# Kernel optimization log

Hardware: AMD Instinct MI355X
Metric: run time of the kernel (lower is better)

## Reference

```python
import jax, jax.numpy as jnp
import numpy as np

EPS = 1e-6


def layernorm(x, w, b):
    m = jnp.mean(x, axis=-1, keepdims=True)
    v = jnp.var(x, axis=-1, keepdims=True)
    return (x - m) * jax.lax.rsqrt(v + EPS) * w + b


def rotate_half(x):
    x1, x2 = jnp.split(x, 2, axis=-1)
    return jnp.concatenate((-x2, x1), axis=-1)


def setup_inputs() -> dict:
    key = jax.random.key(0)
    ks = jax.random.split(key, 16)
    T, D, H, HD, I = 16384, 1280, 16, 80, 5120
    NSEG = 16
    inp = {
        "hidden_states": jax.random.normal(ks[0], (T, D), jnp.float32),
        "cos": jax.random.uniform(ks[1], (T, HD), jnp.float32),
        "sin": jax.random.uniform(ks[2], (T, HD), jnp.float32),
        "ln1_w": jnp.ones((D,), jnp.float32),
        "ln1_b": jnp.zeros((D,), jnp.float32),
        "ln2_w": jnp.ones((D,), jnp.float32),
        "ln2_b": jnp.zeros((D,), jnp.float32),
        "qkv_w": jax.random.normal(ks[3], (3 * D, D), jnp.float32) * 0.02,
        "qkv_b": jnp.zeros((3 * D,), jnp.float32),
        "proj_w": jax.random.normal(ks[4], (D, D), jnp.float32) * 0.02,
        "proj_b": jnp.zeros((D,), jnp.float32),
        "fc1_w": jax.random.normal(ks[5], (I, D), jnp.float32) * 0.02,
        "fc1_b": jnp.zeros((I,), jnp.float32),
        "fc2_w": jax.random.normal(ks[6], (D, I), jnp.float32) * 0.02,
        "fc2_b": jnp.zeros((D,), jnp.float32),
        "cu_seqlens": jnp.arange(NSEG + 1, dtype=jnp.int32) * (T // NSEG),
    }
    return inp


def reference(hidden_states, cos, sin, ln1_w, ln1_b, ln2_w, ln2_b,
              qkv_w, qkv_b, proj_w, proj_b, fc1_w, fc1_b, fc2_w, fc2_b,
              cu_seqlens):
    T, D = hidden_states.shape
    H = 16
    HD = D // H
    nseg = cu_seqlens.shape[0] - 1  # equal-length segments by construction
    L = T // nseg

    x = layernorm(hidden_states, ln1_w, ln1_b)
    qkv = (x @ qkv_w.T + qkv_b).reshape(T, 3, H, HD)
    q, k, v = qkv[:, 0], qkv[:, 1], qkv[:, 2]  # [T, H, HD]

    # RoPE in fp32, cos/sin broadcast over heads
    c = cos[:, None, :]
    s = sin[:, None, :]
    q = q * c + rotate_half(q) * s
    k = k * c + rotate_half(k) * s

    # block-diagonal varlen attention: reshape into [nseg, L, H, HD]
    qs = q.reshape(nseg, L, H, HD)
    ks = k.reshape(nseg, L, H, HD)
    vs = v.reshape(nseg, L, H, HD)
    scale = 1.0 / jnp.sqrt(jnp.asarray(HD, jnp.float32))
    scores = jnp.einsum('slhd,smhd->shlm', qs, ks) * scale
    probs = jax.nn.softmax(scores, axis=-1)
    attn = jnp.einsum('shlm,smhd->slhd', probs, vs).reshape(T, D)

    attn_out = attn @ proj_w.T + proj_b
    h = hidden_states + attn_out

    y = layernorm(h, ln2_w, ln2_b)
    mlp = (jax.nn.silu(y @ fc1_w.T + fc1_b)) @ fc2_w.T + fc2_b
    return h + mlp
```

## Files before the change

### kernel.cpp

```cpp
#include <hip/hip_runtime.h>
#include <hip/hip_bf16.h>
#include <hip/hip_fp16.h>

typedef _Float16 f16;
typedef _Float16 f16x4 __attribute__((ext_vector_type(4)));
typedef _Float16 f16x8 __attribute__((ext_vector_type(8)));
typedef float f32x4 __attribute__((ext_vector_type(4)));

#define T_TOK 16384
#define D_MOD 1280
#define N_QKV 3840
#define I_MLP 5120
#define N_HEAD 16
#define HD 80
#define SEG_L 1024

__device__ __forceinline__ void async16(const void* g, void* l) {
    __builtin_amdgcn_global_load_lds(
        (const __attribute__((address_space(1))) void*)g,
        (__attribute__((address_space(3))) void*)l, 16, 0, 0);
}

__global__ __launch_bounds__(256) void cast_f32_f16(
    const float* __restrict__ src, f16* __restrict__ dst, int n) {
    int i = blockIdx.x * 256 + threadIdx.x;
    if (i < n) dst[i] = (f16)src[i];
}

template <typename TIN>
__global__ __launch_bounds__(256) void ln_kernel(
    const TIN* __restrict__ x, const float* __restrict__ w,
    const float* __restrict__ b, f16* __restrict__ out) {
    const int t = blockIdx.x;
    const TIN* row = x + (size_t)t * D_MOD;
    float vals[5];
    float s = 0.f, s2 = 0.f;
    for (int i = 0; i < 5; ++i) {
        float v = (float)row[threadIdx.x + i * 256];
        vals[i] = v; s += v; s2 += v * v;
    }
    for (int off = 32; off > 0; off >>= 1) {
        s  += __shfl_down(s, off);
        s2 += __shfl_down(s2, off);
    }
    __shared__ float rs[4], rs2[4];
    int wv = threadIdx.x >> 6;
    if ((threadIdx.x & 63) == 0) { rs[wv] = s; rs2[wv] = s2; }
    __syncthreads();
    s  = rs[0] + rs[1] + rs[2] + rs[3];
    s2 = rs2[0] + rs2[1] + rs2[2] + rs2[3];
    float m = s * (1.f / D_MOD);
    float var = s2 * (1.f / D_MOD) - m * m;
    float rstd = rsqrtf(var + 1e-6f);
    for (int i = 0; i < 5; ++i) {
        int c = threadIdx.x + i * 256;
        out[(size_t)t * D_MOD + c] = (f16)((vals[i] - m) * rstd * w[c] + b[c]);
    }
}

__global__ __launch_bounds__(256) void rope_inplace(
    f16* __restrict__ q, f16* __restrict__ k,
    const float* __restrict__ cosb, const float* __restrict__ sinb) {
    int i = blockIdx.x * 256 + threadIdx.x;
    if (i >= T_TOK * N_HEAD * 40) return;
    int d = i % 40;
    int th = i / 40;
    int h = th & 15;
    int t = th >> 4;
    size_t i0 = ((size_t)h * T_TOK + t) * HD + d;
    size_t i1 = i0 + 40;
    float c0 = cosb[t * HD + d],      s0 = sinb[t * HD + d];
    float c1 = cosb[t * HD + d + 40], s1 = sinb[t * HD + d + 40];
    {
        float x0 = (float)q[i0], x1 = (float)q[i1];
        q[i0] = (f16)(x0 * c0 - x1 * s0);
        q[i1] = (f16)(x1 * c1 + x0 * s1);
    }
    {
        float x0 = (float)k[i0], x1 = (float)k[i1];
        k[i0] = (f16)(x0 * c0 - x1 * s0);
        k[i1] = (f16)(x1 * c1 + x0 * s1);
    }
}

#define EPI_QKV   0
#define EPI_PROJ  1
#define EPI_SILU  2
#define EPI_FC2A  3
#define EPI_FC2B  4

template <int EPI>
__global__ __launch_bounds__(256, 2) void gemm_bt(
    const f16* __restrict__ A, const f16* __restrict__ B,
    const float* __restrict__ bias, const void* __restrict__ resid,
    void* __restrict__ out0, f16* __restrict__ out1, f16* __restrict__ out2,
    int M, int N, int K, int lda, int ldb, int ldo) {
    __shared__ f16 lA[128 * 32];
    __shared__ f16 lB[128 * 32];
    const int tid = threadIdx.x;
    const int w = tid >> 6, l = tid & 63;
    const int wr = w >> 1, wc = w & 1;
    const int lane16 = l & 15, quad = l >> 4;
    const int m0 = blockIdx.y * 128, n0 = blockIdx.x * 128;
    const int rowA = l >> 2;
    const int colA = (l & 3) * 8;

    f32x4 acc[4][4];
    for (int i = 0; i < 4; ++i)
        for (int j = 0; j < 4; ++j)
            acc[i][j] = (f32x4){0.f, 0.f, 0.f, 0.f};

    for (int k0 = 0; k0 < K; k0 += 32) {
        __syncthreads();
        for (int p = 0; p < 2; ++p) {
            int r = p * 64 + w * 16;
            async16(A + (size_t)(m0 + r + rowA) * lda + k0 + colA, &lA[r * 32]);
            async16(B + (size_t)(n0 + r + rowA) * ldb + k0 + colA, &lB[r * 32]);
        }
        __syncthreads();
        f16x8 af[4], bf[4];
        for (int i = 0; i < 4; ++i) {
            af[i] = *(const f16x8*)&lA[(wr * 64 + i * 16 + lane16) * 32 + quad * 8];
            bf[i] = *(const f16x8*)&lB[(wc * 64 + i * 16 + lane16) * 32 + quad * 8];
        }
        for (int mi = 0; mi < 4; ++mi)
            for (int ni = 0; ni < 4; ++ni)
                acc[mi][ni] = __builtin_amdgcn_mfma_f32_16x16x32_f16(
                    af[mi], bf[ni], acc[mi][ni], 0, 0, 0);
    }

    for (int mi = 0; mi < 4; ++mi) {
        int row = m0 + wr * 64 + mi * 16 + quad * 4;
        for (int ni = 0; ni < 4; ++ni) {
            int col = n0 + wc * 64 + ni * 16 + lane16;
            float bv = (EPI == EPI_FC2B) ? 0.f : bias[col];
            if (EPI == EPI_QKV) {
                int g = col / D_MOD;
                int rem = col - g * D_MOD;
                int h = rem / HD, d = rem - h * HD;
                if (g == 2) {
                    f16x4 pk;
                    for (int r2 = 0; r2 < 4; ++r2)
                        pk[r2] = (f16)(acc[mi][ni][r2] + bv);
                    f16* dst = out2 + ((size_t)h * HD + d) * T_TOK + row;
                    *(f16x4*)dst = pk;
                } else {
                    f16* dst = (g == 0) ? (f16*)out0 : out1;
                    size_t base = ((size_t)h * T_TOK) * HD + d;
                    for (int r2 = 0; r2 < 4; ++r2) {
                        float v = acc[mi][ni][r2] + bv;
                        dst[base + (size_t)(row + r2) * HD] = (f16)v;
                    }
                }
            } else {
                for (int r2 = 0; r2 < 4; ++r2) {
                    float v = acc[mi][ni][r2] + bv;
                    size_t idx = (size_t)(row + r2) * ldo + col;
                    if (EPI == EPI_PROJ) {
                        ((f16*)out0)[idx] = (f16)(v + ((const float*)resid)[idx]);
                    } else if (EPI == EPI_SILU) {
                        ((f16*)out0)[idx] = (f16)(v / (1.f + __expf(-v)));
                    } else if (EPI == EPI_FC2A) {
                        ((float*)out0)[idx] = v + (float)((const f16*)resid)[idx];
                    } else {
                        ((float*)out0)[idx] += v;
                    }
                }
            }
        }
    }
}

#define QK_STRIDE 104
#define VT_STRIDE 72
#define P_STRIDE  72
__global__ __launch_bounds__(256, 3) void attn_kernel(
    const f16* __restrict__ q, const f16* __restrict__ k,
    const f16* __restrict__ vt, f16* __restrict__ out) {
    const int bid = blockIdx.x;
    const int s = bid >> 8, h = (bid >> 4) & 15, qt = bid & 15;
    const int t0 = s * SEG_L;
    __shared__ f16 lQ[64 * QK_STRIDE];
    __shared__ f16 lK[64 * QK_STRIDE];
    __shared__ f16 lVt[80 * VT_STRIDE];
    __shared__ f16 lP[4 * 16 * P_STRIDE];
    const int tid = threadIdx.x;
    const int w = tid >> 6, l = tid & 63;
    const int lane16 = l & 15, quad = l >> 4;
    const f16 scale = (f16)0.16132167f;

    const f16* qbase  = q  + (size_t)h * T_TOK * HD + (size_t)(t0 + qt * 64) * HD;
    const f16* kbase  = k  + (size_t)h * T_TOK * HD + (size_t)t0 * HD;
    const f16* vtbase = vt + (size_t)h * HD * T_TOK + t0;

    for (int idx = tid; idx < 64 * 12; idx += 256) {
        int r = idx / 12, c8 = idx % 12;
        f16x8 val = (f16x8){0, 0, 0, 0, 0, 0, 0, 0};
        if (c8 < 10) {
            val = *(const f16x8*)&qbase[r * 80 + c8 * 8];
            val = val * scale;
        }
        *(f16x8*)&lQ[r * QK_STRIDE + c8 * 8] = val;
    }
    for (int idx = tid; idx < 64 * 2; idx += 256) {
        int r = idx >> 1, c8 = 10 + (idx & 1);
        *(f16x8*)&lK[r * QK_STRIDE + c8 * 8] = (f16x8){0, 0, 0, 0, 0, 0, 0, 0};
    }

    float lrow[4] = {0.f, 0.f, 0.f, 0.f};
    f32x4 o[5];
    for (int i = 0; i < 5; ++i) o[i] = (f32x4){0.f, 0.f, 0.f, 0.f};

    for (int kt = 0; kt < 16; ++kt) {
        __syncthreads();
        for (int idx = tid; idx < 64 * 10; idx += 256) {
            int r = idx / 10, c8 = idx % 10;
            *(f16x8*)&lK[r * QK_STRIDE + c8 * 8] =
                *(const f16x8*)&kbase[(kt * 64 + r) * 80 + c8 * 8];
        }
        for (int idx = tid; idx < 80 * 8; idx += 256) {
            int d = idx / 8, r8 = idx % 8;
            *(f16x8*)&lVt[d * VT_STRIDE + r8 * 8] =
                *(const f16x8*)&vtbase[(size_t)d * T_TOK + kt * 64 + r8 * 8];
        }
        __syncthreads();

        f32x4 sacc[4];
        for (int ct = 0; ct < 4; ++ct) {
            f32x4 a = (f32x4){0.f, 0.f, 0.f, 0.f};
            for (int ks = 0; ks < 3; ++ks) {
                f16x8 af = *(const f16x8*)&lQ[(w * 16 + lane16) * QK_STRIDE + ks * 32 + quad * 8];
                f16x8 bf = *(const f16x8*)&lK[(ct * 16 + lane16) * QK_STRIDE + ks * 32 + quad * 8];
                a = __builtin_amdgcn_mfma_f32_16x16x32_f16(af, bf, a, 0, 0, 0);
            }
            sacc[ct] = a;
        }

        for (int ct = 0; ct < 4; ++ct) {
            for (int r = 0; r < 4; ++r) {
                float p = __builtin_exp2f(fminf(sacc[ct][r], 14.f));
                lrow[r] += p;
                lP[w * 16 * P_STRIDE + (quad * 4 + r) * P_STRIDE + ct * 16 + lane16] = (f16)p;
            }
        }

        for (int vt2 = 0; vt2 < 5; ++vt2) {
            for (int ks = 0; ks < 2; ++ks) {
                f16x8 af = *(const f16x8*)&lP[w * 16 * P_STRIDE + lane16 * P_STRIDE + ks * 32 + quad * 8];
                f16x8 bf = *(const f16x8*)&lVt[(vt2 * 16 + lane16) * VT_STRIDE + ks * 32 + quad * 8];
                o[vt2] = __builtin_amdgcn_mfma_f32_16x16x32_f16(af, bf, o[vt2], 0, 0, 0);
            }
        }
    }

    for (int r = 0; r < 4; ++r)
        for (int off = 1; off < 16; off <<= 1)
            lrow[r] += __shfl_xor(lrow[r], off);

    f16* obase = out + (size_t)(t0 + qt * 64 + w * 16) * D_MOD + h * HD;
    for (int r = 0; r < 4; ++r) {
        float inv = 1.f / lrow[r];
        for (int vt2 = 0; vt2 < 5; ++vt2) {
            int row = quad * 4 + r;
            int hd = vt2 * 16 + lane16;
            obase[(size_t)row * D_MOD + hd] = (f16)(o[vt2][r] * inv);
        }
    }
}

extern "C" void kernel_launch(void* const* d_in, const int* in_sizes, int n_in,
                              void* d_out, int out_size, void* d_ws, size_t ws_size,
                              hipStream_t stream) {
    const float* hidden = (const float*)d_in[0];
    const float* cosb   = (const float*)d_in[1];
    const float* sinb   = (const float*)d_in[2];
    const float* ln1w   = (const float*)d_in[3];
    const float* ln1b   = (const float*)d_in[4];
    const float* ln2w   = (const float*)d_in[5];
    const float* ln2b   = (const float*)d_in[6];
    const float* qkvw   = (const float*)d_in[7];
    const float* qkvb   = (const float*)d_in[8];
    const float* projw  = (const float*)d_in[9];
    const float* projb  = (const float*)d_in[10];
    const float* fc1w   = (const float*)d_in[11];
    const float* fc1b   = (const float*)d_in[12];
    const float* fc2w   = (const float*)d_in[13];
    const float* fc2b   = (const float*)d_in[14];
    float* out = (float*)d_out;

    f16* wqkv  = (f16*)d_ws;
    f16* wproj = wqkv  + 4915200;
    f16* wfc1  = wproj + 1638400;
    f16* wfc2  = wfc1  + 6553600;
    f16* qf    = wfc2  + 6553600;
    f16* kf    = qf    + 20971520;
    f16* vf    = kf    + 20971520;
    f16* xf    = vf    + 20971520;
    f16* hbuf  = xf    + 20971520;
    f16* attnf  = xf;
    f16* yf     = qf;
    f16* fc1out = kf;

    cast_f32_f16<<<(4915200 + 255) / 256, 256, 0, stream>>>(qkvw, wqkv, 4915200);
    cast_f32_f16<<<(1638400 + 255) / 256, 256, 0, stream>>>(projw, wproj, 1638400);
    cast_f32_f16<<<(6553600 + 255) / 256, 256, 0, stream>>>(fc1w, wfc1, 6553600);
    cast_f32_f16<<<(6553600 + 255) / 256, 256, 0, stream>>>(fc2w, wfc2, 6553600);

    ln_kernel<float><<<T_TOK, 256, 0, stream>>>(hidden, ln1w, ln1b, xf);

    gemm_bt<EPI_QKV><<<dim3(N_QKV / 128, T_TOK / 128), 256, 0, stream>>>(
        xf, wqkv, qkvb, nullptr, qf, kf, vf,
        T_TOK, N_QKV, D_MOD, D_MOD, D_MOD, 0);

    rope_inplace<<<(T_TOK * N_HEAD * 40) / 256, 256, 0, stream>>>(qf, kf, cosb, sinb);

    attn_kernel<<<16 * 16 * 16, 256, 0, stream>>>(qf, kf, vf, attnf);

    gemm_bt<EPI_PROJ><<<dim3(D_MOD / 128, T_TOK / 128), 256, 0, stream>>>(
        attnf, wproj, projb, hidden, hbuf, nullptr, nullptr,
        T_TOK, D_MOD, D_MOD, D_MOD, D_MOD, D_MOD);

    ln_kernel<f16><<<T_TOK, 256, 0, stream>>>(hbuf, ln2w, ln2b, yf);

    for (int c = 0; c < 2; ++c) {
        gemm_bt<EPI_SILU><<<dim3(2560 / 128, T_TOK / 128), 256, 0, stream>>>(
            yf, wfc1 + (size_t)c * 2560 * D_MOD, fc1b + c * 2560, nullptr,
            fc1out, nullptr, nullptr,
            T_TOK, 2560, D_MOD, D_MOD, D_MOD, 2560);
        if (c == 0) {
            gemm_bt<EPI_FC2A><<<dim3(D_MOD / 128, T_TOK / 128), 256, 0, stream>>>(
                fc1out, wfc2, fc2b, hbuf, out, nullptr, nullptr,
                T_TOK, D_MOD, 2560, 2560, I_MLP, D_MOD);
        } else {
            gemm_bt<EPI_FC2B><<<dim3(D_MOD / 128, T_TOK / 128), 256, 0, stream>>>(
                fc1out, wfc2 + 2560, fc2b, nullptr, out, nullptr, nullptr,
                T_TOK, D_MOD, 2560, 2560, I_MLP, D_MOD);
        }
    }
}
```

Baseline: 1.668 ms.

## Rewrite GEMM as 256x256 tile, 8-wave kernel with double-buffered async LDS pipeline

Replaces the 128x128, 4-wave GEMM with a 256x256 tile processed by 8 waves. K steps of 64 are double-buffered in XOR-swizzled LDS and loaded asynchronously, with global loads for later stages interleaved between four MFMA quadrant phases. It also remaps workgroups to tiles to improve L2 locality and raises MFMA priority with setprio. The aim is to hide global-load latency and cut LDS bank conflicts and per-step barrier stalls. In exchange it uses much more LDS and registers, and relies on hand-written barrier and waitcnt ordering.

New measurement: 1.509 ms. -9.5%, faster.

```diff
diff --git a/kernel.cpp b/kernel.cpp
--- a/kernel.cpp
+++ b/kernel.cpp
@@ -20,6 +20,11 @@
         (const __attribute__((address_space(1))) void*)g,
         (__attribute__((address_space(3))) void*)l, 16, 0, 0);
 }
+
+#define BAR()        asm volatile("s_barrier" ::: "memory")
+#define WAIT_LGKM0() do { asm volatile("s_waitcnt lgkmcnt(0)" ::: "memory"); \
+                          __builtin_amdgcn_sched_barrier(0); } while (0)
+#define WAIT_VM(n)   asm volatile("s_waitcnt vmcnt(" #n ")" ::: "memory")
 
 __global__ __launch_bounds__(256) void cast_f32_f16(
     const float* __restrict__ src, f16* __restrict__ dst, int n) {
@@ -89,50 +94,131 @@
 #define EPI_FC2A  3
 #define EPI_FC2B  4
 
+#define READ_A(MH) \
+    _Pragma("unroll") for (int mi = 0; mi < 4; ++mi) { \
+        const f16* pa = &LB[lb][MH][(wr * 64 + mi * 16 + lane16) * 64]; \
+        aF[mi][0] = *(const f16x8*)&pa[ch0]; \
+        aF[mi][1] = *(const f16x8*)&pa[ch1]; \
+    }
+#define READ_B(NH) \
+    _Pragma("unroll") for (int ni = 0; ni < 2; ++ni) { \
+        const f16* pb = &LB[lb][2 + NH][(wc * 32 + ni * 16 + lane16) * 64]; \
+        bF[ni][0] = *(const f16x8*)&pb[ch0]; \
+        bF[ni][1] = *(const f16x8*)&pb[ch1]; \
+    }
+#define DO_MFMA(MH, NH) \
+    __builtin_amdgcn_s_setprio(1); \
+    _Pragma("unroll") for (int mi = 0; mi < 4; ++mi) \
+    _Pragma("unroll") for (int ni = 0; ni < 2; ++ni) { \
+        acc[MH][NH][mi][ni] = __builtin_amdgcn_mfma_f32_16x16x32_f16( \
+            aF[mi][0], bF[ni][0], acc[MH][NH][mi][ni], 0, 0, 0); \
+        acc[MH][NH][mi][ni] = __builtin_amdgcn_mfma_f32_16x16x32_f16( \
+            aF[mi][1], bF[ni][1], acc[MH][NH][mi][ni], 0, 0, 0); \
+    } \
+    __builtin_amdgcn_s_setprio(0);
+
 template <int EPI>
-__global__ __launch_bounds__(256, 2) void gemm_bt(
+__global__ __launch_bounds__(512, 2) void gemm_bt(
     const f16* __restrict__ A, const f16* __restrict__ B,
     const float* __restrict__ bias, const void* __restrict__ resid,
     void* __restrict__ out0, f16* __restrict__ out1, f16* __restrict__ out2,
     int M, int N, int K, int lda, int ldb, int ldo) {
-    __shared__ f16 lA[128 * 32];
-    __shared__ f16 lB[128 * 32];
+    __shared__ __align__(16) f16 LB[2][4][8192];
     const int tid = threadIdx.x;
-    const int w = tid >> 6, l = tid & 63;
-    const int wr = w >> 1, wc = w & 1;
+    const int w = tid >> 6;
+    const int l = tid & 63;
     const int lane16 = l & 15, quad = l >> 4;
-    const int m0 = blockIdx.y * 128, n0 = blockIdx.x * 128;
-    const int rowA = l >> 2;
-    const int colA = (l & 3) * 8;
-
-    f32x4 acc[4][4];
-    for (int i = 0; i < 4; ++i)
-        for (int j = 0; j < 4; ++j)
-            acc[i][j] = (f32x4){0.f, 0.f, 0.f, 0.f};
-
-    for (int k0 = 0; k0 < K; k0 += 32) {
-        __syncthreads();
-        for (int p = 0; p < 2; ++p) {
-            int r = p * 64 + w * 16;
-            async16(A + (size_t)(m0 + r + rowA) * lda + k0 + colA, &lA[r * 32]);
-            async16(B + (size_t)(n0 + r + rowA) * ldb + k0 + colA, &lB[r * 32]);
-        }
-        __syncthreads();
-        f16x8 af[4], bf[4];
-        for (int i = 0; i < 4; ++i) {
-            af[i] = *(const f16x8*)&lA[(wr * 64 + i * 16 + lane16) * 32 + quad * 8];
-            bf[i] = *(const f16x8*)&lB[(wc * 64 + i * 16 + lane16) * 32 + quad * 8];
-        }
-        for (int mi = 0; mi < 4; ++mi)
-            for (int ni = 0; ni < 4; ++ni)
-                acc[mi][ni] = __builtin_amdgcn_mfma_f32_16x16x32_f16(
-                    af[mi], bf[ni], acc[mi][ni], 0, 0, 0);
-    }
-
+    const int wr = w >> 2, wc = w & 3;
+
+    const int nx = gridDim.x;
+    int id = blockIdx.y * nx + blockIdx.x;
+    const int nwg = nx * gridDim.y;
+    int tile = ((nwg & 7) == 0) ? ((id & 7) * (nwg >> 3) + (id >> 3)) : id;
+    const int m0 = (tile / nx) * 256;
+    const int n0 = (tile % nx) * 256;
+    const int NT = K >> 6;
+
+    const int rr = tid >> 3;
+    const int cc = (tid & 7) ^ (rr & 7);
+    const size_t ga_off = (size_t)rr * lda + cc * 8;
+    const size_t gb_off = (size_t)rr * ldb + cc * 8;
+    const int lds_off = w * 512;
+    const int swz = lane16 & 7;
+    const int ch0 = ((0 * 4 + quad) ^ swz) * 8;
+    const int ch1 = ((1 * 4 + quad) ^ swz) * 8;
+
+    f32x4 acc[2][2][4][2];
+#pragma unroll
+    for (int a = 0; a < 2; ++a)
+#pragma unroll
+        for (int b2 = 0; b2 < 2; ++b2)
+#pragma unroll
+            for (int c = 0; c < 4; ++c)
+#pragma unroll
+                for (int d = 0; d < 2; ++d)
+                    acc[a][b2][c][d] = (f32x4){0.f, 0.f, 0.f, 0.f};
+
+    const f16* Abase = A + (size_t)m0 * lda;
+    const f16* Bbase = B + (size_t)n0 * ldb;
+    auto stageA = [&](int buf, int ph, int t) {
+        const f16* g = Abase + (size_t)(ph * 128) * lda + (size_t)t * 64 + ga_off;
+        f16* lr = &LB[buf][ph][0] + lds_off;
+        async16(g, lr);
+        async16(g + (size_t)64 * lda, lr + 4096);
+    };
+    auto stageB = [&](int buf, int ph, int t) {
+        const f16* g = Bbase + (size_t)(ph * 128) * ldb + (size_t)t * 64 + gb_off;
+        f16* lr = &LB[buf][2 + ph][0] + lds_off;
+        async16(g, lr);
+        async16(g + (size_t)64 * ldb, lr + 4096);
+    };
+
+    stageA(0, 0, 0); stageB(0, 1, 0); stageA(0, 1, 0); stageB(0, 0, 0);
+    if (NT > 1) {
+        stageA(1, 0, 1); stageB(1, 1, 1); stageA(1, 1, 1);
+        WAIT_VM(6);
+    } else {
+        WAIT_VM(0);
+    }
+    BAR();
+
+    for (int t = 0; t < NT; ++t) {
+        const int lb = t & 1;
+        f16x8 aF[4][2], bF[2][2];
+        READ_A(0); READ_B(0);
+        { int tau = t + 1; if (tau < NT) stageB(tau & 1, 0, tau); }
+        BAR(); WAIT_LGKM0();
+        DO_MFMA(0, 0);
+        BAR();
+        READ_B(1);
+        { int tau = t + 2; if (tau < NT) stageA(tau & 1, 0, tau); }
+        BAR(); WAIT_LGKM0();
+        DO_MFMA(0, 1);
+        BAR();
+        READ_A(1);
+        { int tau = t + 2; if (tau < NT) stageB(tau & 1, 1, tau); }
+        BAR(); WAIT_LGKM0();
+        DO_MFMA(1, 1);
+        BAR();
+        READ_B(0);
+        { int tau = t + 2; if (tau < NT) stageA(tau & 1, 1, tau); }
+        BAR(); WAIT_LGKM0();
+        DO_MFMA(1, 0);
+        if (t < NT - 2) { WAIT_VM(6); } else { WAIT_VM(0); }
+        BAR();
+    }
+
+#pragma unroll
+    for (int mh = 0; mh < 2; ++mh)
+#pragma unroll
     for (int mi = 0; mi < 4; ++mi) {
-        int row = m0 + wr * 64 + mi * 16 + quad * 4;
-        for (int ni = 0; ni < 4; ++ni) {
-            int col = n0 + wc * 64 + ni * 16 + lane16;
+        const int row = m0 + mh * 128 + wr * 64 + mi * 16 + quad * 4;
+#pragma unroll
+        for (int nh = 0; nh < 2; ++nh)
+#pragma unroll
+        for (int ni = 0; ni < 2; ++ni) {
+            const int col = n0 + nh * 128 + wc * 32 + ni * 16 + lane16;
+            const f32x4 v4 = acc[mh][nh][mi][ni];
             float bv = (EPI == EPI_FC2B) ? 0.f : bias[col];
             if (EPI == EPI_QKV) {
                 int g = col / D_MOD;
@@ -140,21 +226,23 @@
                 int h = rem / HD, d = rem - h * HD;
                 if (g == 2) {
                     f16x4 pk;
-                    for (int r2 = 0; r2 < 4; ++r2)
-                        pk[r2] = (f16)(acc[mi][ni][r2] + bv);
+#pragma unroll
+                    for (int r2 = 0; r2 < 4; ++r2) pk[r2] = (f16)(v4[r2] + bv);
                     f16* dst = out2 + ((size_t)h * HD + d) * T_TOK + row;
                     *(f16x4*)dst = pk;
                 } else {
                     f16* dst = (g == 0) ? (f16*)out0 : out1;
                     size_t base = ((size_t)h * T_TOK) * HD + d;
+#pragma unroll
                     for (int r2 = 0; r2 < 4; ++r2) {
-                        float v = acc[mi][ni][r2] + bv;
+                        float v = v4[r2] + bv;
                         dst[base + (size_t)(row + r2) * HD] = (f16)v;
                     }
                 }
             } else {
+#pragma unroll
                 for (int r2 = 0; r2 < 4; ++r2) {
-                    float v = acc[mi][ni][r2] + bv;
+                    float v = v4[r2] + bv;
                     size_t idx = (size_t)(row + r2) * ldo + col;
                     if (EPI == EPI_PROJ) {
                         ((f16*)out0)[idx] = (f16)(v + ((const float*)resid)[idx]);
@@ -170,6 +258,10 @@
         }
     }
 }
+
+#undef READ_A
+#undef READ_B
+#undef DO_MFMA
 
 #define QK_STRIDE 104
 #define VT_STRIDE 72
@@ -308,7 +400,7 @@
 
     ln_kernel<float><<<T_TOK, 256, 0, stream>>>(hidden, ln1w, ln1b, xf);
 
-    gemm_bt<EPI_QKV><<<dim3(N_QKV / 128, T_TOK / 128), 256, 0, stream>>>(
+    gemm_bt<EPI_QKV><<<dim3(N_QKV / 256, T_TOK / 256), 512, 0, stream>>>(
         xf, wqkv, qkvb, nullptr, qf, kf, vf,
         T_TOK, N_QKV, D_MOD, D_MOD, D_MOD, 0);
 
@@ -316,23 +408,23 @@
 
     attn_kernel<<<16 * 16 * 16, 256, 0, stream>>>(qf, kf, vf, attnf);
 
-    gemm_bt<EPI_PROJ><<<dim3(D_MOD / 128, T_TOK / 128), 256, 0, stream>>>(
+    gemm_bt<EPI_PROJ><<<dim3(D_MOD / 256, T_TOK / 256), 512, 0, stream>>>(
         attnf, wproj, projb, hidden, hbuf, nullptr, nullptr,
         T_TOK, D_MOD, D_MOD, D_MOD, D_MOD, D_MOD);
 
     ln_kernel<f16><<<T_TOK, 256, 0, stream>>>(hbuf, ln2w, ln2b, yf);
 
     for (int c = 0; c < 2; ++c) {
-        gemm_bt<EPI_SILU><<<dim3(2560 / 128, T_TOK / 128), 256, 0, stream>>>(
+        gemm_bt<EPI_SILU><<<dim3(2560 / 256, T_TOK / 256), 512, 0, stream>>>(
             yf, wfc1 + (size_t)c * 2560 * D_MOD, fc1b + c * 2560, nullptr,
             fc1out, nullptr, nullptr,
             T_TOK, 2560, D_MOD, D_MOD, D_MOD, 2560);
         if (c == 0) {
-            gemm_bt<EPI_FC2A><<<dim3(D_MOD / 128, T_TOK / 128), 256, 0, stream>>>(
+            gemm_bt<EPI_FC2A><<<dim3(D_MOD / 256, T_TOK / 256), 512, 0, stream>>>(
                 fc1out, wfc2, fc2b, hbuf, out, nullptr, nullptr,
                 T_TOK, D_MOD, 2560, 2560, I_MLP, D_MOD);
         } else {
-            gemm_bt<EPI_FC2B><<<dim3(D_MOD / 128, T_TOK / 128), 256, 0, stream>>>(
+            gemm_bt<EPI_FC2B><<<dim3(D_MOD / 256, T_TOK / 256), 512, 0, stream>>>(
                 fc1out, wfc2 + 2560, fc2b, nullptr, out, nullptr, nullptr,
                 T_TOK, D_MOD, 2560, 2560, I_MLP, D_MOD);
         }
```
